# Performance work log

Hardware: AMD Instinct MI355X
Metric: run time of the kernel (lower is better)

The kernel has to match this reference:

```python
import jax, jax.numpy as jnp
import numpy as np

D_MODEL = 64
N_HEADS = 4
HEAD_DIM = D_MODEL // N_HEADS  # 16
D_FF = 4 * D_MODEL  # 256
LN_EPS = 1e-5


def _layer_norm(x, g, b):
    mu = jnp.mean(x, axis=-1, keepdims=True)
    var = jnp.var(x, axis=-1, keepdims=True)
    return (x - mu) * jax.lax.rsqrt(var + LN_EPS) * g + b


def setup_inputs() -> dict:
    key = jax.random.key(0)
    ks = jax.random.split(key, 16)
    B, S = 4, 2048
    s = 0.05
    return {
        "x": jax.random.normal(ks[0], (B, S, D_MODEL), dtype=jnp.float32),
        # per-head projection weights (stacked over the head axis)
        "wq": jax.random.normal(ks[1], (N_HEADS, D_MODEL, HEAD_DIM), dtype=jnp.float32) * s,
        "bq": jax.random.normal(ks[2], (N_HEADS, HEAD_DIM), dtype=jnp.float32) * s,
        "wk": jax.random.normal(ks[3], (N_HEADS, D_MODEL, HEAD_DIM), dtype=jnp.float32) * s,
        "bk": jax.random.normal(ks[4], (N_HEADS, HEAD_DIM), dtype=jnp.float32) * s,
        "wv": jax.random.normal(ks[5], (N_HEADS, D_MODEL, HEAD_DIM), dtype=jnp.float32) * s,
        "bv": jax.random.normal(ks[6], (N_HEADS, HEAD_DIM), dtype=jnp.float32) * s,
        "wo": jax.random.normal(ks[7], (D_MODEL, D_MODEL), dtype=jnp.float32) * s,
        "bo": jax.random.normal(ks[8], (D_MODEL,), dtype=jnp.float32) * s,
        "ln1_g": jnp.ones((D_MODEL,), dtype=jnp.float32),
        "ln1_b": jnp.zeros((D_MODEL,), dtype=jnp.float32),
        "w1": jax.random.normal(ks[9], (D_MODEL, D_FF), dtype=jnp.float32) * s,
        "b1": jax.random.normal(ks[10], (D_FF,), dtype=jnp.float32) * s,
        "w2": jax.random.normal(ks[11], (D_FF, D_MODEL), dtype=jnp.float32) * s,
        "b2": jax.random.normal(ks[12], (D_MODEL,), dtype=jnp.float32) * s,
        "ln2_g": jnp.ones((D_MODEL,), dtype=jnp.float32),
        "ln2_b": jnp.zeros((D_MODEL,), dtype=jnp.float32),
    }


def reference(x, wq, bq, wk, bk, wv, bv, wo, bo, ln1_g, ln1_b, w1, b1, w2, b2, ln2_g, ln2_b):
    B, S, _ = x.shape
    # per-head projections, vectorized over the head axis
    Q = jnp.einsum('bsd,hdk->bhsk', x, wq) + bq[None, :, None, :]
    K = jnp.einsum('bsd,hdk->bhsk', x, wk) + bk[None, :, None, :]
    V = jnp.einsum('bsd,hdk->bhsk', x, wv) + bv[None, :, None, :]
    # scaled causal attention (mask materialized as in the original)
    scores = jnp.einsum('bhsk,bhtk->bhst', Q, K) / jnp.sqrt(jnp.float32(HEAD_DIM))
    causal = jnp.tril(jnp.ones((S, S), dtype=bool))  # keep lower triangle
    scores = jnp.where(causal, scores, -jnp.inf)
    attn = jax.nn.softmax(scores, axis=-1)
    A = jnp.einsum('bhst,bhtk->bhsk', attn, V)
    # concat heads -> [B, S, D]
    A = A.transpose(0, 2, 1, 3).reshape(B, S, D_MODEL)
    out = A @ wo + bo
    out = out + x
    out = _layer_norm(out, ln1_g, ln1_b)
    ff = jnp.maximum(out @ w1 + b1, 0.0) @ w2 + b2  # dropout is identity in eval
    out = _layer_norm(ff + out, ln2_g, ln2_b)
    return out
```

## Files before the change

### kernel.cpp

```cpp
#include <hip/hip_runtime.h>

#define DEVFN __device__ __forceinline__

constexpr int B = 4, S = 2048, H = 4, DH = 16, D = 64, F = 256;
constexpr int T = B * S;
constexpr int PAIRS = B * H;
constexpr int CPP = 72;
constexpr int NZ = PAIRS * CPP;
constexpr int PSTRIDE = 1280;
constexpr float LOG2E = 1.44269504f;

typedef __attribute__((ext_vector_type(8))) short s16x8;
typedef __attribute__((ext_vector_type(16))) float f32x16;
typedef __attribute__((ext_vector_type(4))) float f32x4;

DEVFN float wave_sum(float v) {
#pragma unroll
    for (int mask = 32; mask >= 1; mask >>= 1)
        v += __shfl_xor(v, mask, 64);
    return v;
}

DEVFN float bf2f(unsigned short u) { return __uint_as_float((unsigned)u << 16); }
DEVFN unsigned short f2bf(float f) {
    unsigned b = __float_as_uint(f);
    return (unsigned short)((b + 0x8000u) >> 16);
}
DEVFN unsigned pack_bf2(float lo, float hi) {
    unsigned a = __float_as_uint(lo), b = __float_as_uint(hi);
    return ((a + 0x8000u) >> 16) | ((b + 0x8000u) & 0xffff0000u);
}
DEVFN unsigned cvtpk(float lo, float hi) {
    unsigned r;
    asm("v_cvt_pk_bf16_f32 %0, %1, %2" : "=v"(r) : "v"(lo), "v"(hi));
    return r;
}
DEVFN void plswap(unsigned& a, unsigned& b) {
#if __has_builtin(__builtin_amdgcn_permlane32_swap)
    typedef unsigned uv2 __attribute__((ext_vector_type(2)));
    uv2 r = __builtin_amdgcn_permlane32_swap(a, b, false, false);
    a = r[0]; b = r[1];
#else
    asm volatile("v_permlane32_swap_b32 %0, %1" : "+v"(a), "+v"(b));
#endif
}

__global__ __launch_bounds__(256) void k_qkv(
    const float* __restrict__ x,
    const float* __restrict__ wq, const float* __restrict__ bq,
    const float* __restrict__ wk, const float* __restrict__ bk,
    const float* __restrict__ wv, const float* __restrict__ bv,
    const float* __restrict__ wo, const float* __restrict__ w1,
    const float* __restrict__ w2,
    unsigned short* __restrict__ Qb, unsigned short* __restrict__ Kb,
    unsigned short* __restrict__ Vtg,
    unsigned* __restrict__ wob, unsigned* __restrict__ w1b,
    unsigned* __restrict__ w2b)
{
    __shared__ __align__(16) unsigned short xfr[2][2][64][8];
    __shared__ __align__(16) unsigned short wfr[12][2][64][8];

    int tid = threadIdx.x, lane = tid & 63, w = tid >> 6;
    int t0 = blockIdx.x * 32;
    int b = t0 >> 11;
    int sbase = t0 & (S - 1);

#pragma unroll
    for (int e = 0; e < 4; ++e) {
        int i = e * 256 + tid;
        int tt = i >> 9, ks = (i >> 8) & 1, l = (i >> 2) & 63, ee = 2 * (i & 3);
        int token = 16 * tt + (l & 15);
        int kk = 32 * ks + 8 * (l >> 4) + ee;
        float2 xv = *(const float2*)(x + (size_t)(t0 + token) * D + kk);
        *(unsigned*)&xfr[tt][ks][l][ee] = pack_bf2(xv.x, xv.y);
    }
#pragma unroll
    for (int e = 0; e < 24; ++e) {
        int i = e * 256 + tid;
        int combo = i >> 9, ks = (i >> 8) & 1, l = (i >> 2) & 63, ee = 2 * (i & 3);
        int m = combo >> 2, jt = combo & 3;
        int j15 = l & 15;
        int kk = 32 * ks + 8 * (l >> 4) + ee;
        const float* wsrc = (m == 0) ? wq : (m == 1) ? wk : wv;
        float a = wsrc[jt * 1024 + kk * 16 + j15];
        float c = wsrc[jt * 1024 + (kk + 1) * 16 + j15];
        *(unsigned*)&wfr[combo][ks][l][ee] = pack_bf2(a, c);
    }

    if (blockIdx.x < 16) {
        int bi = blockIdx.x;
        if (tid < 128) {
            int i = bi * 128 + tid;
            int jt = i >> 9, ks = (i >> 8) & 1, l = (i >> 2) & 63, ee = 2 * (i & 3);
            int j = 16 * jt + (l & 15);
            int k = 32 * ks + 8 * (l >> 4) + ee;
            wob[i] = pack_bf2(wo[k * D + j], wo[(k + 1) * D + j]);
        }
#pragma unroll
        for (int e = 0; e < 2; ++e) {
            int i = bi * 512 + e * 256 + tid;
            int ft = i >> 9, ks = (i >> 8) & 1, l = (i >> 2) & 63, ee = 2 * (i & 3);
            int f = 16 * ft + (l & 15);
            int k = 32 * ks + 8 * (l >> 4) + ee;
            w1b[i] = pack_bf2(w1[k * F + f], w1[(k + 1) * F + f]);
        }
#pragma unroll
        for (int e = 0; e < 2; ++e) {
            int i = bi * 512 + e * 256 + tid;
            int jt = i >> 11, ks = (i >> 8) & 7, l = (i >> 2) & 63, ee = 2 * (i & 3);
            int j = 16 * jt + (l & 15);
            int k = 32 * ks + 8 * (l >> 4) + ee;
            w2b[i] = pack_bf2(w2[k * D + j], w2[(k + 1) * D + j]);
        }
    }
    __syncthreads();

    int j15 = lane & 15, q4 = lane >> 4;
#pragma unroll
    for (int t3 = 0; t3 < 3; ++t3) {
        int combo = w * 3 + t3;
        int m = combo >> 2, jt = combo & 3;
        int j = 16 * jt + j15;
        int pair = b * H + jt;
#pragma unroll
        for (int tt = 0; tt < 2; ++tt) {
            f32x4 c = {0.f, 0.f, 0.f, 0.f};
#pragma unroll
            for (int ks = 0; ks < 2; ++ks) {
                s16x8 af = *(const s16x8*)&xfr[tt][ks][lane][0];
                s16x8 bf = *(const s16x8*)&wfr[combo][ks][lane][0];
                c = __builtin_amdgcn_mfma_f32_16x16x32_bf16(af, bf, c, 0, 0, 0);
            }
            int s0 = sbase + 16 * tt + 4 * q4;
            if (m == 0) {
                float bj = bq[j];
#pragma unroll
                for (int r = 0; r < 4; ++r)
                    Qb[((size_t)pair * S + s0 + r) * DH + j15] =
                        f2bf((c[r] + bj) * (0.25f * LOG2E));
            } else if (m == 1) {
                float bj = bk[j];
#pragma unroll
                for (int r = 0; r < 4; ++r)
                    Kb[((size_t)pair * S + s0 + r) * DH + j15] = f2bf(c[r] + bj);
            } else {
                float bj = bv[j];
                uint2 o;
                o.x = pack_bf2(c[0] + bj, c[1] + bj);
                o.y = pack_bf2(c[2] + bj, c[3] + bj);
                *(uint2*)(Vtg + ((size_t)pair * DH + j15) * S + s0) = o;
            }
        }
    }
}

__global__ __launch_bounds__(256) void k_attn_part(
    const unsigned short* __restrict__ Qb, const unsigned short* __restrict__ Kb,
    const unsigned short* __restrict__ Vtg, float* __restrict__ P)
{
    __shared__ unsigned short Kt[256][16];
    __shared__ unsigned short Vt[16][264];

    int tid = threadIdx.x, lane = tid & 63, w = tid >> 6;

    int bid0 = blockIdx.x;
    int z = (bid0 & 7) * 144 + (bid0 >> 3);
    int pair = z / CPP;
    int rem = z - pair * CPP;
    int qb = 0, cum = 0;
    while (cum + (qb >> 1) + 1 <= rem) { cum += (qb >> 1) + 1; ++qb; }
    int kc = rem - cum;
    int kbase = kc << 8;
    int qbase = qb << 7;

    {
        const uint4* src = (const uint4*)(Kb + (size_t)(pair * S + kbase + tid) * DH);
        uint4 lo = src[0], hi = src[1];
        *(uint4*)&Kt[tid][(tid & 1) * 8] = lo;
        *(uint4*)&Kt[tid][((tid & 1) ^ 1) * 8] = hi;
        int r = tid >> 4, cc = tid & 15;
        const uint4* vs = (const uint4*)(Vtg + (size_t)(pair * DH + r) * S + kbase + cc * 16);
        uint4 v0 = vs[0], v1 = vs[1];
        *(uint4*)&Vt[r][cc * 16] = v0;
        *(uint4*)&Vt[r][cc * 16 + 8] = v1;
    }
    __syncthreads();

    int qn = lane & 31, g = lane >> 5;
    int q0w = qbase + w * 32;
    int qg = q0w + qn;
    int vrow = lane & 15;

    s16x8 qf = *(const s16x8*)(Qb + (size_t)(pair * S + qg) * DH + g * 8);

    f32x16 czero;
#pragma unroll
    for (int i = 0; i < 16; ++i) czero[i] = 0.f;
    f32x16 acc = czero;
    float mrun = -1e30f, lsum = 0.f;

    int nt = ((q0w + 31 - kbase) >> 5) + 1;
    if (nt > 8) nt = 8;

    int krow0 = qn;
    s16x8 kf = *(const s16x8*)&Kt[krow0][(g ^ (krow0 & 1)) * 8];

    for (int t = 0; t < nt; ++t) {
        int kl = t * 32;
        s16x8 vf0 = *(const s16x8*)&Vt[vrow][kl + g * 8];
        s16x8 vf1 = *(const s16x8*)&Vt[vrow][kl + 16 + g * 8];
        int tn = (t + 1 < nt) ? (t + 1) : t;
        int krown = tn * 32 + qn;
        s16x8 kfn = *(const s16x8*)&Kt[krown][(g ^ (krown & 1)) * 8];

        f32x16 sc = __builtin_amdgcn_mfma_f32_32x32x16_bf16(kf, qf, czero, 0, 0, 0);
        if (t == nt - 1) {
            int qml = qg - (kbase + kl);
#pragma unroll
            for (int r = 0; r < 16; ++r) {
                int m = (r & 3) + 8 * (r >> 2) + 4 * g;
                sc[r] = (m <= qml) ? sc[r] : -1e30f;
            }
        }
        float t0a = fmaxf(fmaxf(sc[0], sc[1]), sc[2]);
        float t1a = fmaxf(fmaxf(sc[3], sc[4]), sc[5]);
        float t2a = fmaxf(fmaxf(sc[6], sc[7]), sc[8]);
        float t3a = fmaxf(fmaxf(sc[9], sc[10]), sc[11]);
        float t4a = fmaxf(fmaxf(sc[12], sc[13]), sc[14]);
        float tm = fmaxf(fmaxf(fmaxf(t0a, t1a), fmaxf(t2a, t3a)),
                         fmaxf(t4a, sc[15]));
        tm = fmaxf(tm, __shfl_xor(tm, 32, 64));
        float mnew = fmaxf(mrun, tm);
        float scale = exp2f(mrun - mnew);
        mrun = mnew;
        float p[16];
        float ts0 = 0.f, ts1 = 0.f, ts2 = 0.f, ts3 = 0.f;
#pragma unroll
        for (int r = 0; r < 16; r += 4) {
            p[r]     = exp2f(sc[r] - mnew);     ts0 += p[r];
            p[r + 1] = exp2f(sc[r + 1] - mnew); ts1 += p[r + 1];
            p[r + 2] = exp2f(sc[r + 2] - mnew); ts2 += p[r + 2];
            p[r + 3] = exp2f(sc[r + 3] - mnew); ts3 += p[r + 3];
        }
        float ts = (ts0 + ts1) + (ts2 + ts3);
        ts += __shfl_xor(ts, 32, 64);
        lsum = fmaf(lsum, scale, ts);
#pragma unroll
        for (int r = 0; r < 8; ++r) acc[r] *= scale;

        unsigned a0 = cvtpk(p[0],  p[1]);
        unsigned a1 = cvtpk(p[2],  p[3]);
        unsigned a2 = cvtpk(p[4],  p[5]);
        unsigned a3 = cvtpk(p[6],  p[7]);
        unsigned b0 = cvtpk(p[8],  p[9]);
        unsigned b1 = cvtpk(p[10], p[11]);
        unsigned b2 = cvtpk(p[12], p[13]);
        unsigned b3 = cvtpk(p[14], p[15]);
        plswap(a0, a2);
        plswap(a1, a3);
        plswap(b0, b2);
        plswap(b1, b3);
        union UU { unsigned u[4]; s16x8 v; };
        UU pf0, pf1;
        pf0.u[0] = a0; pf0.u[1] = a1; pf0.u[2] = a2; pf0.u[3] = a3;
        pf1.u[0] = b0; pf1.u[1] = b1; pf1.u[2] = b2; pf1.u[3] = b3;

        acc = __builtin_amdgcn_mfma_f32_32x32x16_bf16(vf0, pf0.v, acc, 0, 0, 0);
        acc = __builtin_amdgcn_mfma_f32_32x32x16_bf16(vf1, pf1.v, acc, 0, 0, 0);
        kf = kfn;
    }

    float* base = P + (size_t)z * PSTRIDE;
    if (lane < 32) {
        base[w * 32 + qn] = mrun;
        base[128 + w * 32 + qn] = lsum;
    }
    uint2 cA, cB;
    cA.x = pack_bf2(acc[0], acc[1]); cA.y = pack_bf2(acc[2], acc[3]);
    cB.x = pack_bf2(acc[4], acc[5]); cB.y = pack_bf2(acc[6], acc[7]);
    unsigned short* pa = (unsigned short*)(base + 256);
    *(uint2*)&pa[(w * 32 + qn) * 16 + 4 * g] = cA;
    *(uint2*)&pa[(w * 32 + qn) * 16 + 8 + 4 * g] = cB;
}

__global__ __launch_bounds__(256) void k_post(
    const float* __restrict__ P, const float* __restrict__ x,
    const unsigned* __restrict__ wob, const float* __restrict__ bo,
    const float* __restrict__ g1, const float* __restrict__ bb1,
    const unsigned* __restrict__ w1b, const float* __restrict__ b1,
    const unsigned* __restrict__ w2b, const float* __restrict__ b2,
    const float* __restrict__ g2, const float* __restrict__ bb2,
    float* __restrict__ out)
{
    __shared__ unsigned short Asb[16][72];
    __shared__ float Os[16][68];
    __shared__ float R1s[16][68];
    __shared__ unsigned short R1sb[16][72];
    __shared__ unsigned short Hhb[16][264];

    int tid = threadIdx.x, lane = tid & 63, w = tid >> 6;
    int t0 = blockIdx.x * 16;
    int b = t0 >> 11;
    int sbase = t0 & (S - 1);
    int qb = sbase >> 7;
    int nc = (qb >> 1) + 1;
    int cum = 0;
#pragma unroll
    for (int i = 0; i < 16; ++i) cum += (i < qb) ? ((i >> 1) + 1) : 0;

    {
        int token = tid >> 4, sub = tid & 15;
        int h = sub >> 2, dq = sub & 3;
        int pair = b * H + h;
        int q = (sbase & 127) + token;
        const float* base0 = P + ((size_t)pair * CPP + cum) * PSTRIDE;

        float mv[8], sv[8]; uint2 uv[8];
#pragma unroll
        for (int c = 0; c < 8; ++c) {
            int cc = (c < nc) ? c : (nc - 1);
            const float* bc = base0 + cc * PSTRIDE;
            float m_ = bc[q];
            float s_ = bc[128 + q];
            uint2 u_ = *(const uint2*)((const unsigned*)(bc + 256) + q * 8 + dq * 2);
            bool valid = (c < nc);
            mv[c] = valid ? m_ : -1e30f;
            sv[c] = valid ? s_ : 0.f;
            uv[c].x = valid ? u_.x : 0u;
            uv[c].y = valid ? u_.y : 0u;
        }
        float M = fmaxf(fmaxf(fmaxf(mv[0], mv[1]), fmaxf(mv[2], mv[3])),
                        fmaxf(fmaxf(mv[4], mv[5]), fmaxf(mv[6], mv[7])));
        float Sm = 0.f, a0 = 0.f, a1 = 0.f, a2 = 0.f, a3 = 0.f;
#pragma unroll
        for (int c = 0; c < 8; ++c) {
            float e = exp2f(mv[c] - M);
            Sm = fmaf(sv[c], e, Sm);
            a0 = fmaf(__uint_as_float(uv[c].x << 16), e, a0);
            a1 = fmaf(__uint_as_float(uv[c].x & 0xffff0000u), e, a1);
            a2 = fmaf(__uint_as_float(uv[c].y << 16), e, a2);
            a3 = fmaf(__uint_as_float(uv[c].y & 0xffff0000u), e, a3);
        }
        float inv = 1.f / Sm;
        uint2 o;
        o.x = cvtpk(a0 * inv, a1 * inv);
        o.y = cvtpk(a2 * inv, a3 * inv);
        *(uint2*)&Asb[token][16 * h + 4 * dq] = o;
    }
    __syncthreads();

    {
        f32x4 c = {0.f, 0.f, 0.f, 0.f};
#pragma unroll
        for (int ks = 0; ks < 2; ++ks) {
            s16x8 af = *(const s16x8*)&Asb[lane & 15][32 * ks + 8 * (lane >> 4)];
            s16x8 bf = *(const s16x8*)(wob + (((w * 2) + ks) * 64 + lane) * 4);
            c = __builtin_amdgcn_mfma_f32_16x16x32_bf16(af, bf, c, 0, 0, 0);
        }
        int j = 16 * w + (lane & 15);
        int q4 = lane >> 4;
        float boj = bo[j];
#pragma unroll
        for (int r = 0; r < 4; ++r) {
            int tk = q4 * 4 + r;
            Os[tk][j] = c[r] + boj + x[(size_t)(t0 + tk) * D + j];
        }
    }
    __syncthreads();

    {
        int j = lane;
        float gj = g1[j], bj = bb1[j];
#pragma unroll
        for (int i = 0; i < 4; ++i) {
            int tk = w * 4 + i;
            float o = Os[tk][j];
            float mu = wave_sum(o) * (1.f / 64.f);
            float dif = o - mu;
            float var = wave_sum(dif * dif) * (1.f / 64.f);
            float r1 = dif * rsqrtf(var + 1e-5f) * gj + bj;
            R1s[tk][j] = r1;
            R1sb[tk][j] = f2bf(r1);
        }
    }
    __syncthreads();

    {
        int q4 = lane >> 4;
#pragma unroll
        for (int t = 0; t < 4; ++t) {
            int ft = w * 4 + t;
            f32x4 c = {0.f, 0.f, 0.f, 0.f};
#pragma unroll
            for (int ks = 0; ks < 2; ++ks) {
                s16x8 af = *(const s16x8*)&R1sb[lane & 15][32 * ks + 8 * (lane >> 4)];
                s16x8 bf = *(const s16x8*)(w1b + (((ft * 2) + ks) * 64 + lane) * 4);
                c = __builtin_amdgcn_mfma_f32_16x16x32_bf16(af, bf, c, 0, 0, 0);
            }
            int f = 16 * ft + (lane & 15);
            float b1f = b1[f];
#pragma unroll
            for (int r = 0; r < 4; ++r)
                Hhb[q4 * 4 + r][f] = f2bf(fmaxf(c[r] + b1f, 0.f));
        }
    }
    __syncthreads();

    {
        f32x4 c = {0.f, 0.f, 0.f, 0.f};
#pragma unroll
        for (int ks = 0; ks < 8; ++ks) {
            s16x8 af = *(const s16x8*)&Hhb[lane & 15][32 * ks + 8 * (lane >> 4)];
            s16x8 bf = *(const s16x8*)(w2b + (((w * 8) + ks) * 64 + lane) * 4);
            c = __builtin_amdgcn_mfma_f32_16x16x32_bf16(af, bf, c, 0, 0, 0);
        }
        int j = 16 * w + (lane & 15);
        int q4 = lane >> 4;
        float b2j = b2[j];
#pragma unroll
        for (int r = 0; r < 4; ++r) {
            int tk = q4 * 4 + r;
            Os[tk][j] = c[r] + b2j + R1s[tk][j];
        }
    }
    __syncthreads();

    {
        int j = lane;
        float gj = g2[j], bj = bb2[j];
#pragma unroll
        for (int i = 0; i < 4; ++i) {
            int tk = w * 4 + i;
            float y = Os[tk][j];
            float mu = wave_sum(y) * (1.f / 64.f);
            float dif = y - mu;
            float var = wave_sum(dif * dif) * (1.f / 64.f);
            out[(size_t)(t0 + tk) * D + j] = dif * rsqrtf(var + 1e-5f) * gj + bj;
        }
    }
}

extern "C" void kernel_launch(void* const* d_in, const int* in_sizes, int n_in,
                              void* d_out, int out_size, void* d_ws, size_t ws_size,
                              hipStream_t stream)
{
    const float* x   = (const float*)d_in[0];
    const float* wq  = (const float*)d_in[1];
    const float* bq  = (const float*)d_in[2];
    const float* wk  = (const float*)d_in[3];
    const float* bk  = (const float*)d_in[4];
    const float* wv  = (const float*)d_in[5];
    const float* bv  = (const float*)d_in[6];
    const float* wo  = (const float*)d_in[7];
    const float* bo  = (const float*)d_in[8];
    const float* g1  = (const float*)d_in[9];
    const float* be1 = (const float*)d_in[10];
    const float* w1  = (const float*)d_in[11];
    const float* b1  = (const float*)d_in[12];
    const float* w2  = (const float*)d_in[13];
    const float* b2  = (const float*)d_in[14];
    const float* g2  = (const float*)d_in[15];
    const float* be2 = (const float*)d_in[16];

    char* base = (char*)d_ws;
    unsigned short* Qb  = (unsigned short*)base;
    unsigned short* Kb  = (unsigned short*)(base + (1u << 20));
    unsigned short* Vtg = (unsigned short*)(base + (2u << 20));
    float*          P   = (float*)(base + (3u << 20));
    unsigned*       wob = (unsigned*)(base + (9u << 20));
    unsigned*       w1b = (unsigned*)(base + (9u << 20) + 0x10000);
    unsigned*       w2b = (unsigned*)(base + (9u << 20) + 0x20000);

    k_qkv      <<<T / 32, 256, 0, stream>>>(x, wq, bq, wk, bk, wv, bv,
                                            wo, w1, w2, Qb, Kb, Vtg,
                                            wob, w1b, w2b);
    k_attn_part<<<NZ, 256, 0, stream>>>(Qb, Kb, Vtg, P);
    k_post     <<<T / 16, 256, 0, stream>>>(P, x, wob, bo, g1, be1,
                                            w1b, b1, w2b, b2, g2, be2,
                                            (float*)d_out);
}
```

Before: 38.94 us.

## Process two key tiles per iteration and skip softmax rescale unless max grows

The attention inner loop now handles 64 keys per iteration, issuing two independent QK MFMAs and four PV MFMAs, which halves the number of max/sum/shuffle reductions and gives the scheduler more independent work. It also adds a lazy rescale: the running max and the accumulator rescale are updated only when some lane's tile max exceeds the running max by more than 8 (in log2 units), otherwise exponentials use the stale max. This cuts exp2 and multiply work at the cost of more registers and a possible odd-tile-count read of an extra masked key block. Lazy rescaling allows probabilities up to 2^8 before conversion to bf16.

Result: faster. 37.58 us (-3.5%).

```diff
diff --git a/kernel.cpp b/kernel.cpp
--- a/kernel.cpp
+++ b/kernel.cpp
@@ -201,73 +201,96 @@
 
     int nt = ((q0w + 31 - kbase) >> 5) + 1;
     if (nt > 8) nt = 8;
-
-    int krow0 = qn;
-    s16x8 kf = *(const s16x8*)&Kt[krow0][(g ^ (krow0 & 1)) * 8];
-
-    for (int t = 0; t < nt; ++t) {
-        int kl = t * 32;
-        s16x8 vf0 = *(const s16x8*)&Vt[vrow][kl + g * 8];
-        s16x8 vf1 = *(const s16x8*)&Vt[vrow][kl + 16 + g * 8];
-        int tn = (t + 1 < nt) ? (t + 1) : t;
-        int krown = tn * 32 + qn;
-        s16x8 kfn = *(const s16x8*)&Kt[krown][(g ^ (krown & 1)) * 8];
-
-        f32x16 sc = __builtin_amdgcn_mfma_f32_32x32x16_bf16(kf, qf, czero, 0, 0, 0);
-        if (t == nt - 1) {
-            int qml = qg - (kbase + kl);
+    int ntt = (nt + 1) >> 1;
+
+    for (int u = 0; u < ntt; ++u) {
+        int kl = u * 64;
+        int krowA = kl + qn, krowB = kl + 32 + qn;
+        s16x8 kf0 = *(const s16x8*)&Kt[krowA][(g ^ (krowA & 1)) * 8];
+        s16x8 kf1 = *(const s16x8*)&Kt[krowB][(g ^ (krowB & 1)) * 8];
+        s16x8 vfa0 = *(const s16x8*)&Vt[vrow][kl + g * 8];
+        s16x8 vfa1 = *(const s16x8*)&Vt[vrow][kl + 16 + g * 8];
+        s16x8 vfb0 = *(const s16x8*)&Vt[vrow][kl + 32 + g * 8];
+        s16x8 vfb1 = *(const s16x8*)&Vt[vrow][kl + 48 + g * 8];
+
+        f32x16 sc0 = __builtin_amdgcn_mfma_f32_32x32x16_bf16(kf0, qf, czero, 0, 0, 0);
+        f32x16 sc1 = __builtin_amdgcn_mfma_f32_32x32x16_bf16(kf1, qf, czero, 0, 0, 0);
+
+        if (u == ntt - 1) {
+            int qml0 = qg - (kbase + kl);
+            int qml1 = qml0 - 32;
 #pragma unroll
             for (int r = 0; r < 16; ++r) {
                 int m = (r & 3) + 8 * (r >> 2) + 4 * g;
-                sc[r] = (m <= qml) ? sc[r] : -1e30f;
+                sc0[r] = (m <= qml0) ? sc0[r] : -1e30f;
+                sc1[r] = (m <= qml1) ? sc1[r] : -1e30f;
             }
         }
-        float t0a = fmaxf(fmaxf(sc[0], sc[1]), sc[2]);
-        float t1a = fmaxf(fmaxf(sc[3], sc[4]), sc[5]);
-        float t2a = fmaxf(fmaxf(sc[6], sc[7]), sc[8]);
-        float t3a = fmaxf(fmaxf(sc[9], sc[10]), sc[11]);
-        float t4a = fmaxf(fmaxf(sc[12], sc[13]), sc[14]);
-        float tm = fmaxf(fmaxf(fmaxf(t0a, t1a), fmaxf(t2a, t3a)),
-                         fmaxf(t4a, sc[15]));
+        float mx[8];
+#pragma unroll
+        for (int r = 0; r < 8; ++r)
+            mx[r] = fmaxf(fmaxf(sc0[r], sc0[r + 8]), fmaxf(sc1[r], sc1[r + 8]));
+        float tm = fmaxf(fmaxf(fmaxf(mx[0], mx[1]), fmaxf(mx[2], mx[3])),
+                         fmaxf(fmaxf(mx[4], mx[5]), fmaxf(mx[6], mx[7])));
         tm = fmaxf(tm, __shfl_xor(tm, 32, 64));
-        float mnew = fmaxf(mrun, tm);
-        float scale = exp2f(mrun - mnew);
-        mrun = mnew;
-        float p[16];
+
+        if (__any(tm > mrun + 8.f)) {
+            float mnew = fmaxf(mrun, tm);
+            float scale = exp2f(mrun - mnew);
+            mrun = mnew;
+            lsum *= scale;
+#pragma unroll
+            for (int r = 0; r < 8; ++r) acc[r] *= scale;
+        }
         float ts0 = 0.f, ts1 = 0.f, ts2 = 0.f, ts3 = 0.f;
 #pragma unroll
         for (int r = 0; r < 16; r += 4) {
-            p[r]     = exp2f(sc[r] - mnew);     ts0 += p[r];
-            p[r + 1] = exp2f(sc[r + 1] - mnew); ts1 += p[r + 1];
-            p[r + 2] = exp2f(sc[r + 2] - mnew); ts2 += p[r + 2];
-            p[r + 3] = exp2f(sc[r + 3] - mnew); ts3 += p[r + 3];
+            sc0[r]     = exp2f(sc0[r] - mrun);     ts0 += sc0[r];
+            sc0[r + 1] = exp2f(sc0[r + 1] - mrun); ts1 += sc0[r + 1];
+            sc0[r + 2] = exp2f(sc0[r + 2] - mrun); ts2 += sc0[r + 2];
+            sc0[r + 3] = exp2f(sc0[r + 3] - mrun); ts3 += sc0[r + 3];
+        }
+#pragma unroll
+        for (int r = 0; r < 16; r += 4) {
+            sc1[r]     = exp2f(sc1[r] - mrun);     ts0 += sc1[r];
+            sc1[r + 1] = exp2f(sc1[r + 1] - mrun); ts1 += sc1[r + 1];
+            sc1[r + 2] = exp2f(sc1[r + 2] - mrun); ts2 += sc1[r + 2];
+            sc1[r + 3] = exp2f(sc1[r + 3] - mrun); ts3 += sc1[r + 3];
         }
         float ts = (ts0 + ts1) + (ts2 + ts3);
         ts += __shfl_xor(ts, 32, 64);
-        lsum = fmaf(lsum, scale, ts);
-#pragma unroll
-        for (int r = 0; r < 8; ++r) acc[r] *= scale;
-
-        unsigned a0 = cvtpk(p[0],  p[1]);
-        unsigned a1 = cvtpk(p[2],  p[3]);
-        unsigned a2 = cvtpk(p[4],  p[5]);
-        unsigned a3 = cvtpk(p[6],  p[7]);
-        unsigned b0 = cvtpk(p[8],  p[9]);
-        unsigned b1 = cvtpk(p[10], p[11]);
-        unsigned b2 = cvtpk(p[12], p[13]);
-        unsigned b3 = cvtpk(p[14], p[15]);
-        plswap(a0, a2);
-        plswap(a1, a3);
-        plswap(b0, b2);
-        plswap(b1, b3);
+        lsum += ts;
+
+        unsigned a0 = cvtpk(sc0[0],  sc0[1]);
+        unsigned a1 = cvtpk(sc0[2],  sc0[3]);
+        unsigned a2 = cvtpk(sc0[4],  sc0[5]);
+        unsigned a3 = cvtpk(sc0[6],  sc0[7]);
+        unsigned b0 = cvtpk(sc0[8],  sc0[9]);
+        unsigned b1 = cvtpk(sc0[10], sc0[11]);
+        unsigned b2 = cvtpk(sc0[12], sc0[13]);
+        unsigned b3 = cvtpk(sc0[14], sc0[15]);
+        plswap(a0, a2); plswap(a1, a3); plswap(b0, b2); plswap(b1, b3);
+        unsigned c0 = cvtpk(sc1[0],  sc1[1]);
+        unsigned c1 = cvtpk(sc1[2],  sc1[3]);
+        unsigned c2 = cvtpk(sc1[4],  sc1[5]);
+        unsigned c3 = cvtpk(sc1[6],  sc1[7]);
+        unsigned d0 = cvtpk(sc1[8],  sc1[9]);
+        unsigned d1 = cvtpk(sc1[10], sc1[11]);
+        unsigned d2 = cvtpk(sc1[12], sc1[13]);
+        unsigned d3 = cvtpk(sc1[14], sc1[15]);
+        plswap(c0, c2); plswap(c1, c3); plswap(d0, d2); plswap(d1, d3);
+
         union UU { unsigned u[4]; s16x8 v; };
-        UU pf0, pf1;
+        UU pf0, pf1, pf2, pf3;
         pf0.u[0] = a0; pf0.u[1] = a1; pf0.u[2] = a2; pf0.u[3] = a3;
         pf1.u[0] = b0; pf1.u[1] = b1; pf1.u[2] = b2; pf1.u[3] = b3;
-
-        acc = __builtin_amdgcn_mfma_f32_32x32x16_bf16(vf0, pf0.v, acc, 0, 0, 0);
-        acc = __builtin_amdgcn_mfma_f32_32x32x16_bf16(vf1, pf1.v, acc, 0, 0, 0);
-        kf = kfn;
+        pf2.u[0] = c0; pf2.u[1] = c1; pf2.u[2] = c2; pf2.u[3] = c3;
+        pf3.u[0] = d0; pf3.u[1] = d1; pf3.u[2] = d2; pf3.u[3] = d3;
+
+        acc = __builtin_amdgcn_mfma_f32_32x32x16_bf16(vfa0, pf0.v, acc, 0, 0, 0);
+        acc = __builtin_amdgcn_mfma_f32_32x32x16_bf16(vfa1, pf1.v, acc, 0, 0, 0);
+        acc = __builtin_amdgcn_mfma_f32_32x32x16_bf16(vfb0, pf2.v, acc, 0, 0, 0);
+        acc = __builtin_amdgcn_mfma_f32_32x32x16_bf16(vfb1, pf3.v, acc, 0, 0, 0);
     }
 
     float* base = P + (size_t)z * PSTRIDE;
```
